# Kernel optimization log

Measured on AMD Instinct MI355X. Metric: run time of the kernel, lower is better.

## Reference

```python
import jax, jax.numpy as jnp
import numpy as np

# Config (matches init_kwargs)
V = 32000      # vocab_size
H = 1024       # hidden_size
NH = 16        # num_heads
NKV = 4        # num_kv_heads
L = 4          # num_layers
FF = 4096      # intermediate_size
MAXPOS = 2048
HD = H // NH   # head_dim = 64
KVD = H * NKV // NH  # kv projection dim = 256
EPS = 1e-5


def setup_inputs() -> dict:
    key = jax.random.key(0)
    ks = iter(jax.random.split(key, 64))
    B, T = 1, 2048
    std = 0.02

    def w(shape):
        return jax.random.normal(next(ks), shape, dtype=jnp.float32) * std

    inp = {
        "input_ids": jax.random.randint(next(ks), (B, T), 0, V),
        "attention_mask": jnp.zeros((B, T), dtype=jnp.float32),
        "tok_emb": w((V, H)),
        "pos_emb": w((MAXPOS, H)),
        # stacked per-layer params; Linear weights stored as [in, out]
        "qW": w((L, H, H)),   "qb": jnp.zeros((L, H)),
        "kW": w((L, H, KVD)), "kb": jnp.zeros((L, KVD)),
        "vW": w((L, H, KVD)), "vb": jnp.zeros((L, KVD)),
        "oW": w((L, H, H)),   "ob": jnp.zeros((L, H)),
        "m1W": w((L, H, FF)), "m1b": jnp.zeros((L, FF)),
        "m2W": w((L, FF, H)), "m2b": jnp.zeros((L, H)),
        "ln1g": jnp.ones((L, H)), "ln1b": jnp.zeros((L, H)),
        "ln2g": jnp.ones((L, H)), "ln2b": jnp.zeros((L, H)),
        "lnfg": jnp.ones((H,)),   "lnfb": jnp.zeros((H,)),
        "headW": w((H, V)),  # head: Linear(H, V, bias=False), stored [in,out]
    }
    return inp


def _layer_norm(x, g, b):
    m = jnp.mean(x, axis=-1, keepdims=True)
    v = jnp.mean(jnp.square(x - m), axis=-1, keepdims=True)
    return (x - m) * jax.lax.rsqrt(v + EPS) * g + b


def _gqa_attn(x, mask, qW, qb, kW, kb, vW, vb, oW, ob):
    B, T, _ = x.shape
    G = NH // NKV  # query groups per kv head
    q = (x @ qW + qb).reshape(B, T, NH, HD).transpose(0, 2, 1, 3)        # [B,NH,T,HD]
    q = q.reshape(B, NKV, G, T, HD)                                      # [B,NKV,G,T,HD]
    k = (x @ kW + kb).reshape(B, T, NKV, HD).transpose(0, 2, 1, 3)       # [B,NKV,T,HD]
    v = (x @ vW + vb).reshape(B, T, NKV, HD).transpose(0, 2, 1, 3)       # [B,NKV,T,HD]
    # naive full score tensor [B,NKV,G,T,T] (as in the original module)
    scores = jnp.einsum("bkgqd,bksd->bkgqs", q, k) / jnp.sqrt(jnp.float32(HD))
    scores = scores + mask[:, None, None, None, :]  # additive mask over keys
    attn = jax.nn.softmax(scores, axis=-1)
    out = jnp.einsum("bkgqs,bksd->bkgqd", attn, v)                       # [B,NKV,G,T,HD]
    out = out.reshape(B, NH, T, HD).transpose(0, 2, 1, 3).reshape(B, T, H)
    return out @ oW + ob


def reference(input_ids, attention_mask, tok_emb, pos_emb,
              qW, qb, kW, kb, vW, vb, oW, ob,
              m1W, m1b, m2W, m2b,
              ln1g, ln1b, ln2g, ln2b, lnfg, lnfb, headW):
    B, T = input_ids.shape
    x = tok_emb[input_ids] + pos_emb[jnp.arange(T)][None, :, :]  # [B,T,H]
    for i in range(L):
        h = _layer_norm(x, ln1g[i], ln1b[i])
        x = x + _gqa_attn(h, attention_mask, qW[i], qb[i], kW[i], kb[i],
                          vW[i], vb[i], oW[i], ob[i])
        h = _layer_norm(x, ln2g[i], ln2b[i])
        h = jax.nn.gelu(h @ m1W[i] + m1b[i], approximate=False) @ m2W[i] + m2b[i]
        x = x + h
    x = _layer_norm(x, lnfg, lnfb)
    logits = x @ headW  # [B,T,V]
    return logits
```

## Files before the change

### kernel.cpp

```cpp
#include <hip/hip_runtime.h>
#include <stdint.h>
#include <math.h>

typedef __attribute__((ext_vector_type(8))) short bf16x8;
typedef __attribute__((ext_vector_type(4))) short bf16x4;
typedef __attribute__((ext_vector_type(4))) float f32x4;

__device__ __forceinline__ short f2bf(float f) {
  unsigned u = __builtin_bit_cast(unsigned, f);
  unsigned r = u + 0x7fffu + ((u >> 16) & 1u);
  return (short)(r >> 16);
}

__device__ __forceinline__ f32x4 mfma16(bf16x8 a, bf16x8 b, f32x4 c) {
  return __builtin_amdgcn_mfma_f32_16x16x32_bf16(a, b, c, 0, 0, 0);
}

__device__ __forceinline__ void gload16(const void* g, void* l) {
  __builtin_amdgcn_global_load_lds((const __attribute__((address_space(1))) void*)g,
                                   (__attribute__((address_space(3))) void*)l, 16, 0, 0);
}

__device__ __forceinline__ int swz(int row, int col) {
  return row * 64 + (((col >> 3) ^ (row & 7)) << 3) + (col & 7);
}

__global__ __launch_bounds__(256) void embed_k(const int* __restrict__ ids,
                                               const float* __restrict__ tok,
                                               const float* __restrict__ pos,
                                               float* __restrict__ x) {
  int row = blockIdx.x, t = threadIdx.x;
  int id = ids[row];
  const float4 a = *reinterpret_cast<const float4*>(tok + (size_t)id * 1024 + t * 4);
  const float4 b = *reinterpret_cast<const float4*>(pos + (size_t)row * 1024 + t * 4);
  float4 o = make_float4(a.x + b.x, a.y + b.y, a.z + b.z, a.w + b.w);
  *reinterpret_cast<float4*>(x + (size_t)row * 1024 + t * 4) = o;
}

__global__ __launch_bounds__(256) void ln_k(const float* __restrict__ x,
                                            const float* __restrict__ gw,
                                            const float* __restrict__ bw,
                                            short* __restrict__ out) {
  int row = blockIdx.x, t = threadIdx.x;
  const float4 v = *reinterpret_cast<const float4*>(x + (size_t)row * 1024 + t * 4);
  float s = v.x + v.y + v.z + v.w;
  float q = v.x * v.x + v.y * v.y + v.z * v.z + v.w * v.w;
#pragma unroll
  for (int o = 32; o > 0; o >>= 1) { s += __shfl_xor(s, o); q += __shfl_xor(q, o); }
  __shared__ float sh[8];
  int w = t >> 6;
  if ((t & 63) == 0) { sh[w] = s; sh[4 + w] = q; }
  __syncthreads();
  float ts = sh[0] + sh[1] + sh[2] + sh[3];
  float tq = sh[4] + sh[5] + sh[6] + sh[7];
  float mean = ts * (1.f / 1024.f);
  float var  = tq * (1.f / 1024.f) - mean * mean;
  float rstd = rsqrtf(var + 1e-5f);
  const float4 gv = *reinterpret_cast<const float4*>(gw + t * 4);
  const float4 bv = *reinterpret_cast<const float4*>(bw + t * 4);
  bf16x4 ov = { f2bf((v.x - mean) * rstd * gv.x + bv.x),
                f2bf((v.y - mean) * rstd * gv.y + bv.y),
                f2bf((v.z - mean) * rstd * gv.z + bv.z),
                f2bf((v.w - mean) * rstd * gv.w + bv.w) };
  *reinterpret_cast<bf16x4*>(out + (size_t)row * 1024 + t * 4) = ov;
}

__global__ __launch_bounds__(256) void tcvt_k(const float* __restrict__ W,
                                              short* __restrict__ Wt,
                                              int N, size_t inStride, size_t outStride,
                                              int rowOff, int ldOut, float scale) {
  __shared__ float T[128][68];
  const float* Win = W + blockIdx.z * inStride;
  short* Wout = Wt + blockIdx.z * outStride;
  const int n0 = blockIdx.x * 64, k0 = blockIdx.y * 128;
  const int t = threadIdx.x;
  const int nc = (t & 15) * 4, kr = t >> 4;
#pragma unroll
  for (int p = 0; p < 8; ++p) {
    const float4 v = *reinterpret_cast<const float4*>(Win + (size_t)(k0 + kr + 16 * p) * N + n0 + nc);
    T[kr + 16 * p][nc + 0] = v.x;
    T[kr + 16 * p][nc + 1] = v.y;
    T[kr + 16 * p][nc + 2] = v.z;
    T[kr + 16 * p][nc + 3] = v.w;
  }
  __syncthreads();
  const int n = t >> 2, ks = (t & 3) * 32;
  short tmp[32];
#pragma unroll
  for (int i = 0; i < 32; ++i) tmp[i] = f2bf(T[ks + i][n] * scale);
  short* op = Wout + (size_t)(rowOff + n0 + n) * ldOut + k0 + ks;
#pragma unroll
  for (int c = 0; c < 4; ++c)
    *reinterpret_cast<bf16x8*>(op + c * 8) = *reinterpret_cast<bf16x8*>(tmp + c * 8);
}

__global__ __launch_bounds__(256) void bqkv_k(const float* __restrict__ qb,
                                              const float* __restrict__ kb,
                                              const float* __restrict__ vb,
                                              float* __restrict__ o) {
  int l = blockIdx.y;
  int c = blockIdx.x * 256 + threadIdx.x;
  float v;
  if (c < 1024) v = qb[l * 1024 + c] * 0.125f;
  else if (c < 1280) v = kb[l * 256 + c - 1024];
  else v = vb[l * 256 + c - 1280];
  o[l * 1536 + c] = v;
}

__global__ __launch_bounds__(256) void vtr_k(const short* __restrict__ v, int vld,
                                             short* __restrict__ vt) {
  __shared__ short T[64][80];
  const int kvh = blockIdx.y;
  const int s0 = blockIdx.x * 64;
  const int t = threadIdx.x;
  const int row = t >> 3, ch = t & 7;
#pragma unroll
  for (int p = 0; p < 2; ++p) {
    int s = row + 32 * p;
    bf16x8 vv = *reinterpret_cast<const bf16x8*>(v + (size_t)(s0 + s) * vld + kvh * 64 + ch * 8);
    *reinterpret_cast<bf16x8*>(&T[s][ch * 8]) = vv;
  }
  __syncthreads();
#pragma unroll
  for (int p = 0; p < 2; ++p) {
    int d = row + 32 * p;
    short tmp[8];
#pragma unroll
    for (int i = 0; i < 8; ++i) tmp[i] = T[ch * 8 + i][d];
    *reinterpret_cast<bf16x8*>(vt + (size_t)(kvh * 64 + d) * 2048 + s0 + ch * 8) =
        *reinterpret_cast<bf16x8*>(tmp);
  }
}

template <int EPI, int XSWZ, int TILE>
__global__ __launch_bounds__(256, 4)
void gemm_bt(const short* __restrict__ A, const short* __restrict__ Wt,
             const float* __restrict__ bias, const float* __restrict__ resid,
             void* __restrict__ out, int M, int N, int K, int nbOff,
             short* __restrict__ vt) {
  constexpr int BN   = (TILE == 0) ? 128 : 64;
  constexpr int WN   = (TILE == 0) ? 64 : 32;
  constexpr int NT   = (TILE == 0) ? 4 : 2;
  constexpr int BISS = (TILE == 0) ? 4 : 2;
  __shared__ short As[128 * 64];
  __shared__ short Bs[BN * 64];
  const int t = threadIdx.x;
  const int lane = t & 63, w = t >> 6;
  const int g = lane >> 4, r = lane & 15;
  const int wr = w >> 1, wc = w & 1;

  int bx = blockIdx.x, by = blockIdx.y;
  if (XSWZ == 1) {
    const int nbx = gridDim.x, nby = gridDim.y, nwg = nbx * nby;
    const int bid = by * nbx + bx;
    const int q = nwg >> 3, rr = nwg & 7;
    const int xcd = bid & 7, loc = bid >> 3;
    const int sw = (xcd < rr ? xcd * (q + 1) : rr * (q + 1) + (xcd - rr) * q) + loc;
    by = sw % nby; bx = sw / nby;
  }
  const int m0 = by * 128, n0 = (bx + nbOff) * BN;

  f32x4 acc[4][NT];
#pragma unroll
  for (int i = 0; i < 4; ++i)
#pragma unroll
    for (int j = 0; j < NT; ++j) { f32x4 z = {0.f, 0.f, 0.f, 0.f}; acc[i][j] = z; }

  const int srow = lane >> 3, sslot = lane & 7;

  for (int k0 = 0; k0 < K; k0 += 64) {
#pragma unroll
    for (int i = 0; i < 4; ++i) {
      const int rowA = w * 32 + i * 8 + srow;
      const int colA = (sslot ^ (srow & 7)) << 3;
      gload16(A + (size_t)(m0 + rowA) * K + k0 + colA, &As[(w * 32 + i * 8) * 64]);
    }
#pragma unroll
    for (int i = 0; i < BISS; ++i) {
      const int rowB = w * (8 * BISS) + i * 8 + srow;
      const int colB = (sslot ^ (srow & 7)) << 3;
      gload16(Wt + (size_t)(n0 + rowB) * K + k0 + colB, &Bs[(w * (8 * BISS) + i * 8) * 64]);
    }
    __syncthreads();
#pragma unroll
    for (int kk = 0; kk < 64; kk += 32) {
      bf16x8 af[4], bfg[NT];
#pragma unroll
      for (int mt = 0; mt < 4; ++mt)
        af[mt] = *reinterpret_cast<const bf16x8*>(&As[swz(wr * 64 + mt * 16 + r, kk + g * 8)]);
#pragma unroll
      for (int nt = 0; nt < NT; ++nt)
        bfg[nt] = *reinterpret_cast<const bf16x8*>(&Bs[swz(wc * WN + nt * 16 + r, kk + g * 8)]);
#pragma unroll
      for (int mt = 0; mt < 4; ++mt)
#pragma unroll
        for (int nt = 0; nt < NT; ++nt)
          acc[mt][nt] = mfma16(af[mt], bfg[nt], acc[mt][nt]);
    }
    __syncthreads();
  }
#pragma unroll
  for (int nt = 0; nt < NT; ++nt) {
    const int col = n0 + wc * WN + nt * 16 + r;
    const float bv = (EPI == 3) ? 0.f : bias[col];
#pragma unroll
    for (int mt = 0; mt < 4; ++mt) {
#pragma unroll
      for (int j = 0; j < 4; ++j) {
        const int row = m0 + wr * 64 + mt * 16 + 4 * g + j;
        const size_t oi = (size_t)row * N + col;
        float vv = acc[mt][nt][j] + bv;
        if (EPI == 0) {
          ((short*)out)[oi] = f2bf(vv);
        } else if (EPI == 1) {
          vv = 0.5f * vv * (1.f + erff(vv * 0.70710678118654752f));
          ((short*)out)[oi] = f2bf(vv);
        } else if (EPI == 2) {
          ((float*)out)[oi] = resid[oi] + vv;
        } else if (EPI == 3) {
          ((float*)out)[oi] = vv;
        } else {
          short bb = f2bf(vv);
          ((short*)out)[oi] = bb;
          if (col >= 1280) vt[(size_t)(col - 1280) * 2048 + row] = bb;
        }
      }
    }
  }
}

template <int EPI>
__global__ __launch_bounds__(256)
void gemm_k(const short* __restrict__ A, const float* __restrict__ W,
            const float* __restrict__ bias, const float* resid, void* out,
            int M, int N, int K, float scale) {
  __shared__ short As[128 * 64];
  __shared__ short Bs[128 * 64];
  const int t = threadIdx.x;
  const int lane = t & 63;
  const int g = lane >> 4, r = lane & 15;
  const int wid = t >> 6, wr = wid >> 1, wc = wid & 1;
  const int m0 = blockIdx.y * 128, n0 = blockIdx.x * 128;
  f32x4 acc[4][4];
#pragma unroll
  for (int i = 0; i < 4; ++i)
#pragma unroll
    for (int j = 0; j < 4; ++j) { f32x4 z = {0.f, 0.f, 0.f, 0.f}; acc[i][j] = z; }
  const int arow = t >> 3, ac = t & 7;
  const int bnn = t >> 1, bkh = t & 1;
  for (int k0 = 0; k0 < K; k0 += 64) {
#pragma unroll
    for (int p = 0; p < 4; ++p) {
      int row = arow + 32 * p;
      bf16x8 av = *reinterpret_cast<const bf16x8*>(A + (size_t)(m0 + row) * K + k0 + ac * 8);
      *reinterpret_cast<bf16x8*>(&As[swz(row, ac * 8)]) = av;
    }
#pragma unroll
    for (int p = 0; p < 8; ++p) {
      int kg = 4 * (bkh + 2 * p);
      const float* wp = W + (size_t)(k0 + kg) * N + n0 + bnn;
      bf16x4 wv = { f2bf(wp[0]), f2bf(wp[(size_t)N]), f2bf(wp[(size_t)2 * N]), f2bf(wp[(size_t)3 * N]) };
      *reinterpret_cast<bf16x4*>(&Bs[swz(bnn, kg)]) = wv;
    }
    __syncthreads();
#pragma unroll
    for (int kk = 0; kk < 64; kk += 32) {
      bf16x8 af[4], bfg[4];
#pragma unroll
      for (int mt = 0; mt < 4; ++mt)
        af[mt] = *reinterpret_cast<const bf16x8*>(&As[swz(wr * 64 + mt * 16 + r, kk + g * 8)]);
#pragma unroll
      for (int nt = 0; nt < 4; ++nt)
        bfg[nt] = *reinterpret_cast<const bf16x8*>(&Bs[swz(wc * 64 + nt * 16 + r, kk + g * 8)]);
#pragma unroll
      for (int mt = 0; mt < 4; ++mt)
#pragma unroll
        for (int nt = 0; nt < 4; ++nt)
          acc[mt][nt] = mfma16(af[mt], bfg[nt], acc[mt][nt]);
    }
    __syncthreads();
  }
#pragma unroll
  for (int nt = 0; nt < 4; ++nt) {
    const int col = n0 + wc * 64 + nt * 16 + r;
    const float bv = (EPI == 3) ? 0.f : bias[col];
#pragma unroll
    for (int mt = 0; mt < 4; ++mt) {
#pragma unroll
      for (int j = 0; j < 4; ++j) {
        const int row = m0 + wr * 64 + mt * 16 + 4 * g + j;
        const size_t oi = (size_t)row * N + col;
        float vv = acc[mt][nt][j] + bv;
        if (EPI == 0) {
          ((short*)out)[oi] = f2bf(vv * scale);
        } else if (EPI == 1) {
          vv = 0.5f * vv * (1.f + erff(vv * 0.70710678118654752f));
          ((short*)out)[oi] = f2bf(vv);
        } else if (EPI == 2) {
          ((float*)out)[oi] = resid[oi] + vv;
        } else {
          ((float*)out)[oi] = vv;
        }
      }
    }
  }
}

__global__ __launch_bounds__(256) void attn_k(const short* __restrict__ q, int qld,
                                              const short* __restrict__ k, int kld,
                                              const short* __restrict__ vt,
                                              const float* __restrict__ mask,
                                              short* __restrict__ o) {
  __shared__ short Ks[2][64 * 64];
  __shared__ short Vs[2][64 * 64];
  const int t = threadIdx.x, lane = t & 63, w = t >> 6;
  const int g = lane >> 4, r = lane & 15;
  const int h = blockIdx.y, qb = blockIdx.x, kvh = h >> 2;
  const int qrow = qb * 64 + w * 16 + r;

  const short* qp = q + (size_t)qrow * qld + h * 64;
  bf16x8 qf0 = *reinterpret_cast<const bf16x8*>(qp + g * 8);
  bf16x8 qf1 = *reinterpret_cast<const bf16x8*>(qp + 32 + g * 8);

  const short* kbase = k + kvh * 64;
  const short* vbase = vt + (size_t)kvh * 64 * 2048;

  f32x4 oacc[4];
#pragma unroll
  for (int i = 0; i < 4; ++i) { f32x4 z = {0.f, 0.f, 0.f, 0.f}; oacc[i] = z; }
  float m_run = -INFINITY, l_run = 0.f;

  const int srow = w * 8 + (lane >> 3), schunk = lane & 7;

#pragma unroll
  for (int p = 0; p < 2; ++p) {
    const int rr = srow + 32 * p;
    const int cc = (schunk ^ (rr & 7)) << 3;
    gload16(kbase + (size_t)rr * kld + cc, (char*)Ks + p * 4096 + w * 1024);
    gload16(vbase + (size_t)rr * 2048 + cc, (char*)Vs + p * 4096 + w * 1024);
  }
  asm volatile("s_waitcnt vmcnt(0)" ::: "memory");
  __syncthreads();

  for (int it = 0; it < 32; ++it) {
    const int cur = it & 1;
    if (it < 31) {
      const int s1 = (it + 1) * 64;
#pragma unroll
      for (int p = 0; p < 2; ++p) {
        const int rr = srow + 32 * p;
        const int cc = (schunk ^ (rr & 7)) << 3;
        gload16(kbase + (size_t)(s1 + rr) * kld + cc,
                (char*)Ks + (cur ^ 1) * 8192 + p * 4096 + w * 1024);
        gload16(vbase + (size_t)rr * 2048 + s1 + cc,
                (char*)Vs + (cur ^ 1) * 8192 + p * 4096 + w * 1024);
      }
    }
    const int s0 = it * 64;
    const short* Kc = Ks[cur];
    const short* Vc = Vs[cur];

    f32x4 sa[4];
#pragma unroll
    for (int st = 0; st < 4; ++st) {
      bf16x8 kf0 = *reinterpret_cast<const bf16x8*>(&Kc[swz(st * 16 + r, g * 8)]);
      bf16x8 kf1 = *reinterpret_cast<const bf16x8*>(&Kc[swz(st * 16 + r, 32 + g * 8)]);
      f32x4 z = {0.f, 0.f, 0.f, 0.f};
      z = mfma16(kf0, qf0, z);
      z = mfma16(kf1, qf1, z);
      sa[st] = z;
    }
    float sv[16];
    float pmax = -INFINITY;
#pragma unroll
    for (int st = 0; st < 4; ++st) {
      const float4 mv = *reinterpret_cast<const float4*>(mask + s0 + st * 16 + 4 * g);
#pragma unroll
      for (int j = 0; j < 4; ++j) {
        float xx = sa[st][j] + ((const float*)&mv)[j];
        sv[st * 4 + j] = xx;
        pmax = fmaxf(pmax, xx);
      }
    }
    pmax = fmaxf(pmax, __shfl_xor(pmax, 16));
    pmax = fmaxf(pmax, __shfl_xor(pmax, 32));
    float m_new = fmaxf(m_run, pmax);
    float corr = __expf(m_run - m_new);
    float psum = 0.f;
    short pb[16];
#pragma unroll
    for (int i = 0; i < 16; ++i) {
      float p = __expf(sv[i] - m_new);
      psum += p;
      pb[i] = f2bf(p);
    }
    psum += __shfl_xor(psum, 16);
    psum += __shfl_xor(psum, 32);
    l_run = l_run * corr + psum;
    m_run = m_new;
#pragma unroll
    for (int dt = 0; dt < 4; ++dt)
#pragma unroll
      for (int j = 0; j < 4; ++j) oacc[dt][j] *= corr;

#pragma unroll
    for (int hs = 0; hs < 2; ++hs) {
      bf16x8 pf = { pb[hs * 8 + 0], pb[hs * 8 + 1], pb[hs * 8 + 2], pb[hs * 8 + 3],
                    pb[hs * 8 + 4], pb[hs * 8 + 5], pb[hs * 8 + 6], pb[hs * 8 + 7] };
#pragma unroll
      for (int dt = 0; dt < 4; ++dt) {
        int d = dt * 16 + r;
        int c1 = 4 * g + 32 * hs;
        bf16x4 va  = *reinterpret_cast<const bf16x4*>(&Vc[swz(d, c1)]);
        bf16x4 vb2 = *reinterpret_cast<const bf16x4*>(&Vc[swz(d, c1 + 16)]);
        bf16x8 vf = { va[0], va[1], va[2], va[3], vb2[0], vb2[1], vb2[2], vb2[3] };
        oacc[dt] = mfma16(vf, pf, oacc[dt]);
      }
    }
    asm volatile("s_waitcnt vmcnt(0)" ::: "memory");
    __syncthreads();
  }
  float inv = 1.f / l_run;
#pragma unroll
  for (int dt = 0; dt < 4; ++dt) {
    bf16x4 ov = { f2bf(oacc[dt][0] * inv), f2bf(oacc[dt][1] * inv),
                  f2bf(oacc[dt][2] * inv), f2bf(oacc[dt][3] * inv) };
    *reinterpret_cast<bf16x4*>(o + (size_t)qrow * 1024 + h * 64 + dt * 16 + 4 * g) = ov;
  }
}

extern "C" void kernel_launch(void* const* d_in, const int* in_sizes, int n_in,
                              void* d_out, int out_size, void* d_ws, size_t ws_size,
                              hipStream_t stream) {
  const int*   ids   = (const int*)d_in[0];
  const float* mask  = (const float*)d_in[1];
  const float* tok   = (const float*)d_in[2];
  const float* pos   = (const float*)d_in[3];
  const float* qW    = (const float*)d_in[4];
  const float* qbias = (const float*)d_in[5];
  const float* kW    = (const float*)d_in[6];
  const float* kbias = (const float*)d_in[7];
  const float* vW    = (const float*)d_in[8];
  const float* vbias = (const float*)d_in[9];
  const float* oW    = (const float*)d_in[10];
  const float* obias = (const float*)d_in[11];
  const float* m1W   = (const float*)d_in[12];
  const float* m1b   = (const float*)d_in[13];
  const float* m2W   = (const float*)d_in[14];
  const float* m2b   = (const float*)d_in[15];
  const float* ln1g  = (const float*)d_in[16];
  const float* ln1b  = (const float*)d_in[17];
  const float* ln2g  = (const float*)d_in[18];
  const float* ln2b  = (const float*)d_in[19];
  const float* lnfg  = (const float*)d_in[20];
  const float* lnfb  = (const float*)d_in[21];
  const float* headW = (const float*)d_in[22];
  float* out = (float*)d_out;

  char* ws = (char*)d_ws;
  float* x   = (float*)ws;
  short* xb  = (short*)(ws + 8388608ull);

  const size_t OFF_QKV  = 12582912ull;
  const size_t OFF_AO   = 18874368ull;
  const size_t OFF_FF   = 23068672ull;
  const size_t OFF_BQ   = 39845888ull;
  const size_t OFF_WQKV = 39870464ull;
  const size_t OFF_WO   = 52453376ull;
  const size_t OFF_WM1  = 60841984ull;
  const size_t OFF_WM2  = 94396416ull;
  const size_t OFF_WH   = 127950848ull;
  const size_t NEED     = 193486848ull;

  if (ws_size >= NEED) {
    short* qkv  = (short*)(ws + OFF_QKV);
    short* ao   = (short*)(ws + OFF_AO);
    short* ff   = (short*)(ws + OFF_FF);
    short* vt   = ff;
    float* bqv  = (float*)(ws + OFF_BQ);
    short* Wqkv = (short*)(ws + OFF_WQKV);
    short* Wo   = (short*)(ws + OFF_WO);
    short* Wm1  = (short*)(ws + OFF_WM1);
    short* Wm2  = (short*)(ws + OFF_WM2);
    short* Wh   = (short*)(ws + OFF_WH);

    tcvt_k<<<dim3(16, 8, 4), 256, 0, stream>>>(qW, Wqkv, 1024, 1048576ull, 1572864ull, 0, 1024, 0.125f);
    tcvt_k<<<dim3(4, 8, 4),  256, 0, stream>>>(kW, Wqkv, 256,  262144ull,  1572864ull, 1024, 1024, 1.f);
    tcvt_k<<<dim3(4, 8, 4),  256, 0, stream>>>(vW, Wqkv, 256,  262144ull,  1572864ull, 1280, 1024, 1.f);
    tcvt_k<<<dim3(16, 8, 4), 256, 0, stream>>>(oW, Wo, 1024, 1048576ull, 1048576ull, 0, 1024, 1.f);
    tcvt_k<<<dim3(64, 8, 4), 256, 0, stream>>>(m1W, Wm1, 4096, 4194304ull, 4194304ull, 0, 1024, 1.f);
    tcvt_k<<<dim3(16, 32, 4), 256, 0, stream>>>(m2W, Wm2, 1024, 4194304ull, 4194304ull, 0, 4096, 1.f);
    tcvt_k<<<dim3(500, 8, 1), 256, 0, stream>>>(headW, Wh, 32000, 0ull, 0ull, 0, 1024, 1.f);
    bqkv_k<<<dim3(6, 4), 256, 0, stream>>>(qbias, kbias, vbias, bqv);

    embed_k<<<2048, 256, 0, stream>>>(ids, tok, pos, x);

    for (int l = 0; l < 4; ++l) {
      short* Wq_l  = Wqkv + (size_t)l * 1536 * 1024;
      short* Wo_l  = Wo   + (size_t)l * 1024 * 1024;
      short* Wm1_l = Wm1  + (size_t)l * 4096 * 1024;
      short* Wm2_l = Wm2  + (size_t)l * 1024 * 4096;

      ln_k<<<2048, 256, 0, stream>>>(x, ln1g + l * 1024, ln1b + l * 1024, xb);
      gemm_bt<4, 0, 1><<<dim3(24, 16), 256, 0, stream>>>(xb, Wq_l, bqv + l * 1536, nullptr,
                                                         qkv, 2048, 1536, 1024, 0, vt);
      attn_k<<<dim3(32, 16), 256, 0, stream>>>(qkv, 1536, qkv + 1024, 1536, vt, mask, ao);
      gemm_bt<2, 0, 1><<<dim3(16, 16), 256, 0, stream>>>(ao, Wo_l, obias + l * 1024, x,
                                                         x, 2048, 1024, 1024, 0, nullptr);
      ln_k<<<2048, 256, 0, stream>>>(x, ln2g + l * 1024, ln2b + l * 1024, xb);
      gemm_bt<1, 1, 0><<<dim3(32, 16), 256, 0, stream>>>(xb, Wm1_l, m1b + l * 4096, nullptr,
                                                         ff, 2048, 4096, 1024, 0, nullptr);
      gemm_bt<2, 1, 1><<<dim3(16, 16), 256, 0, stream>>>(ff, Wm2_l, m2b + l * 1024, x,
                                                         x, 2048, 1024, 4096, 0, nullptr);
    }
    ln_k<<<2048, 256, 0, stream>>>(x, lnfg, lnfb, xb);
    gemm_bt<3, 1, 0><<<dim3(250, 16), 256, 0, stream>>>(xb, Wh, nullptr, nullptr,
                                                        out, 2048, 32000, 1024, 0, nullptr);
  } else {
    short* qbf = (short*)(ws + (12u << 20));
    short* kbf = (short*)(ws + (16u << 20));
    short* vbf = (short*)(ws + (17u << 20));
    short* ao  = (short*)(ws + (18u << 20));
    short* ff  = (short*)(ws + (22u << 20));
    short* vtf = (short*)(ws + (38u << 20));

    embed_k<<<2048, 256, 0, stream>>>(ids, tok, pos, x);
    for (int l = 0; l < 4; ++l) {
      ln_k<<<2048, 256, 0, stream>>>(x, ln1g + l * 1024, ln1b + l * 1024, xb);
      gemm_k<0><<<dim3(8, 16), 256, 0, stream>>>(xb, qW + (size_t)l * 1024 * 1024,
          qbias + l * 1024, nullptr, qbf, 2048, 1024, 1024, 0.125f);
      gemm_k<0><<<dim3(2, 16), 256, 0, stream>>>(xb, kW + (size_t)l * 1024 * 256,
          kbias + l * 256, nullptr, kbf, 2048, 256, 1024, 1.f);
      gemm_k<0><<<dim3(2, 16), 256, 0, stream>>>(xb, vW + (size_t)l * 1024 * 256,
          vbias + l * 256, nullptr, vbf, 2048, 256, 1024, 1.f);
      vtr_k<<<dim3(32, 4), 256, 0, stream>>>(vbf, 256, vtf);
      attn_k<<<dim3(32, 16), 256, 0, stream>>>(qbf, 1024, kbf, 256, vtf, mask, ao);
      gemm_k<2><<<dim3(8, 16), 256, 0, stream>>>(ao, oW + (size_t)l * 1024 * 1024,
          obias + l * 1024, x, x, 2048, 1024, 1024, 1.f);
      ln_k<<<2048, 256, 0, stream>>>(x, ln2g + l * 1024, ln2b + l * 1024, xb);
      gemm_k<1><<<dim3(32, 16), 256, 0, stream>>>(xb, m1W + (size_t)l * 1024 * 4096,
          m1b + l * 4096, nullptr, ff, 2048, 4096, 1024, 1.f);
      gemm_k<2><<<dim3(8, 16), 256, 0, stream>>>(ff, m2W + (size_t)l * 4096 * 1024,
          m2b + l * 1024, x, x, 2048, 1024, 4096, 1.f);
    }
    ln_k<<<2048, 256, 0, stream>>>(x, lnfg, lnfb, xb);
    gemm_k<3><<<dim3(250, 16), 256, 0, stream>>>(xb, headW, nullptr, nullptr, out,
        2048, 32000, 1024, 1.f);
  }
}
```

Measured before the change: 1.191 ms.

## Use one wave per row in LN/embed, vectorize V-transpose stores, retile MLP1 and head GEMMs

LayerNorm and embedding now process four rows per block with one wavefront per row, which removes the shared-memory reduction and the block barrier. The QKV GEMM epilogue packs four bf16 values into one vector store for the transposed V buffer instead of doing scalar scattered stores. The MLP1 GEMM switches to a narrower-tile template with twice as many blocks, and the vocab head GEMM is split into two launches of half the grid using a column offset argument. The retiling trades per-block data reuse for more parallelism, and the split head adds one extra launch.

```diff
diff --git a/kernel.cpp b/kernel.cpp
--- a/kernel.cpp
+++ b/kernel.cpp
@@ -29,40 +29,49 @@
                                                const float* __restrict__ tok,
                                                const float* __restrict__ pos,
                                                float* __restrict__ x) {
-  int row = blockIdx.x, t = threadIdx.x;
-  int id = ids[row];
-  const float4 a = *reinterpret_cast<const float4*>(tok + (size_t)id * 1024 + t * 4);
-  const float4 b = *reinterpret_cast<const float4*>(pos + (size_t)row * 1024 + t * 4);
-  float4 o = make_float4(a.x + b.x, a.y + b.y, a.z + b.z, a.w + b.w);
-  *reinterpret_cast<float4*>(x + (size_t)row * 1024 + t * 4) = o;
+  const int t = threadIdx.x, w = t >> 6, lane = t & 63;
+  const int row = blockIdx.x * 4 + w;
+  const int id = ids[row];
+#pragma unroll
+  for (int i = 0; i < 4; ++i) {
+    const int c = (i * 64 + lane) * 4;
+    const float4 a = *reinterpret_cast<const float4*>(tok + (size_t)id * 1024 + c);
+    const float4 b = *reinterpret_cast<const float4*>(pos + (size_t)row * 1024 + c);
+    float4 o = make_float4(a.x + b.x, a.y + b.y, a.z + b.z, a.w + b.w);
+    *reinterpret_cast<float4*>(x + (size_t)row * 1024 + c) = o;
+  }
 }
 
 __global__ __launch_bounds__(256) void ln_k(const float* __restrict__ x,
                                             const float* __restrict__ gw,
                                             const float* __restrict__ bw,
                                             short* __restrict__ out) {
-  int row = blockIdx.x, t = threadIdx.x;
-  const float4 v = *reinterpret_cast<const float4*>(x + (size_t)row * 1024 + t * 4);
-  float s = v.x + v.y + v.z + v.w;
-  float q = v.x * v.x + v.y * v.y + v.z * v.z + v.w * v.w;
+  const int t = threadIdx.x, w = t >> 6, lane = t & 63;
+  const int row = blockIdx.x * 4 + w;
+  float4 v[4];
+  float s = 0.f, q = 0.f;
+#pragma unroll
+  for (int i = 0; i < 4; ++i) {
+    v[i] = *reinterpret_cast<const float4*>(x + (size_t)row * 1024 + (i * 64 + lane) * 4);
+    s += v[i].x + v[i].y + v[i].z + v[i].w;
+    q += v[i].x * v[i].x + v[i].y * v[i].y + v[i].z * v[i].z + v[i].w * v[i].w;
+  }
 #pragma unroll
   for (int o = 32; o > 0; o >>= 1) { s += __shfl_xor(s, o); q += __shfl_xor(q, o); }
-  __shared__ float sh[8];
-  int w = t >> 6;
-  if ((t & 63) == 0) { sh[w] = s; sh[4 + w] = q; }
-  __syncthreads();
-  float ts = sh[0] + sh[1] + sh[2] + sh[3];
-  float tq = sh[4] + sh[5] + sh[6] + sh[7];
-  float mean = ts * (1.f / 1024.f);
-  float var  = tq * (1.f / 1024.f) - mean * mean;
-  float rstd = rsqrtf(var + 1e-5f);
-  const float4 gv = *reinterpret_cast<const float4*>(gw + t * 4);
-  const float4 bv = *reinterpret_cast<const float4*>(bw + t * 4);
-  bf16x4 ov = { f2bf((v.x - mean) * rstd * gv.x + bv.x),
-                f2bf((v.y - mean) * rstd * gv.y + bv.y),
-                f2bf((v.z - mean) * rstd * gv.z + bv.z),
-                f2bf((v.w - mean) * rstd * gv.w + bv.w) };
-  *reinterpret_cast<bf16x4*>(out + (size_t)row * 1024 + t * 4) = ov;
+  const float mean = s * (1.f / 1024.f);
+  const float var  = q * (1.f / 1024.f) - mean * mean;
+  const float rstd = rsqrtf(var + 1e-5f);
+#pragma unroll
+  for (int i = 0; i < 4; ++i) {
+    const int c = (i * 64 + lane) * 4;
+    const float4 gv = *reinterpret_cast<const float4*>(gw + c);
+    const float4 bv = *reinterpret_cast<const float4*>(bw + c);
+    bf16x4 ov = { f2bf((v[i].x - mean) * rstd * gv.x + bv.x),
+                  f2bf((v[i].y - mean) * rstd * gv.y + bv.y),
+                  f2bf((v[i].z - mean) * rstd * gv.z + bv.z),
+                  f2bf((v[i].w - mean) * rstd * gv.w + bv.w) };
+    *reinterpret_cast<bf16x4*>(out + (size_t)row * 1024 + c) = ov;
+  }
 }
 
 __global__ __launch_bounds__(256) void tcvt_k(const float* __restrict__ W,
@@ -205,9 +214,11 @@
     const float bv = (EPI == 3) ? 0.f : bias[col];
 #pragma unroll
     for (int mt = 0; mt < 4; ++mt) {
+      const int rowb = m0 + wr * 64 + mt * 16 + 4 * g;
+      short vs[4];
 #pragma unroll
       for (int j = 0; j < 4; ++j) {
-        const int row = m0 + wr * 64 + mt * 16 + 4 * g + j;
+        const int row = rowb + j;
         const size_t oi = (size_t)row * N + col;
         float vv = acc[mt][nt][j] + bv;
         if (EPI == 0) {
@@ -222,8 +233,12 @@
         } else {
           short bb = f2bf(vv);
           ((short*)out)[oi] = bb;
-          if (col >= 1280) vt[(size_t)(col - 1280) * 2048 + row] = bb;
+          vs[j] = bb;
         }
+      }
+      if (EPI == 4 && col >= 1280) {
+        bf16x4 pk = { vs[0], vs[1], vs[2], vs[3] };
+        *reinterpret_cast<bf16x4*>(vt + (size_t)(col - 1280) * 2048 + rowb) = pk;
       }
     }
   }
@@ -493,7 +508,7 @@
     tcvt_k<<<dim3(500, 8, 1), 256, 0, stream>>>(headW, Wh, 32000, 0ull, 0ull, 0, 1024, 1.f);
     bqkv_k<<<dim3(6, 4), 256, 0, stream>>>(qbias, kbias, vbias, bqv);
 
-    embed_k<<<2048, 256, 0, stream>>>(ids, tok, pos, x);
+    embed_k<<<512, 256, 0, stream>>>(ids, tok, pos, x);
 
     for (int l = 0; l < 4; ++l) {
       short* Wq_l  = Wqkv + (size_t)l * 1536 * 1024;
@@ -501,21 +516,23 @@
       short* Wm1_l = Wm1  + (size_t)l * 4096 * 1024;
       short* Wm2_l = Wm2  + (size_t)l * 1024 * 4096;
 
-      ln_k<<<2048, 256, 0, stream>>>(x, ln1g + l * 1024, ln1b + l * 1024, xb);
+      ln_k<<<512, 256, 0, stream>>>(x, ln1g + l * 1024, ln1b + l * 1024, xb);
       gemm_bt<4, 0, 1><<<dim3(24, 16), 256, 0, stream>>>(xb, Wq_l, bqv + l * 1536, nullptr,
                                                          qkv, 2048, 1536, 1024, 0, vt);
       attn_k<<<dim3(32, 16), 256, 0, stream>>>(qkv, 1536, qkv + 1024, 1536, vt, mask, ao);
       gemm_bt<2, 0, 1><<<dim3(16, 16), 256, 0, stream>>>(ao, Wo_l, obias + l * 1024, x,
                                                          x, 2048, 1024, 1024, 0, nullptr);
-      ln_k<<<2048, 256, 0, stream>>>(x, ln2g + l * 1024, ln2b + l * 1024, xb);
-      gemm_bt<1, 1, 0><<<dim3(32, 16), 256, 0, stream>>>(xb, Wm1_l, m1b + l * 4096, nullptr,
+      ln_k<<<512, 256, 0, stream>>>(x, ln2g + l * 1024, ln2b + l * 1024, xb);
+      gemm_bt<1, 1, 1><<<dim3(64, 16), 256, 0, stream>>>(xb, Wm1_l, m1b + l * 4096, nullptr,
                                                          ff, 2048, 4096, 1024, 0, nullptr);
       gemm_bt<2, 1, 1><<<dim3(16, 16), 256, 0, stream>>>(ff, Wm2_l, m2b + l * 1024, x,
                                                          x, 2048, 1024, 4096, 0, nullptr);
     }
-    ln_k<<<2048, 256, 0, stream>>>(x, lnfg, lnfb, xb);
-    gemm_bt<3, 1, 0><<<dim3(250, 16), 256, 0, stream>>>(xb, Wh, nullptr, nullptr,
+    ln_k<<<512, 256, 0, stream>>>(x, lnfg, lnfb, xb);
+    gemm_bt<3, 1, 0><<<dim3(125, 16), 256, 0, stream>>>(xb, Wh, nullptr, nullptr,
                                                         out, 2048, 32000, 1024, 0, nullptr);
+    gemm_bt<3, 1, 0><<<dim3(125, 16), 256, 0, stream>>>(xb, Wh, nullptr, nullptr,
+                                                        out, 2048, 32000, 1024, 125, nullptr);
   } else {
     short* qbf = (short*)(ws + (12u << 20));
     short* kbf = (short*)(ws + (16u << 20));
@@ -524,9 +541,9 @@
     short* ff  = (short*)(ws + (22u << 20));
     short* vtf = (short*)(ws + (38u << 20));
 
-    embed_k<<<2048, 256, 0, stream>>>(ids, tok, pos, x);
+    embed_k<<<512, 256, 0, stream>>>(ids, tok, pos, x);
     for (int l = 0; l < 4; ++l) {
-      ln_k<<<2048, 256, 0, stream>>>(x, ln1g + l * 1024, ln1b + l * 1024, xb);
+      ln_k<<<512, 256, 0, stream>>>(x, ln1g + l * 1024, ln1b + l * 1024, xb);
       gemm_k<0><<<dim3(8, 16), 256, 0, stream>>>(xb, qW + (size_t)l * 1024 * 1024,
           qbias + l * 1024, nullptr, qbf, 2048, 1024, 1024, 0.125f);
       gemm_k<0><<<dim3(2, 16), 256, 0, stream>>>(xb, kW + (size_t)l * 1024 * 256,
@@ -537,13 +554,13 @@
       attn_k<<<dim3(32, 16), 256, 0, stream>>>(qbf, 1024, kbf, 256, vtf, mask, ao);
       gemm_k<2><<<dim3(8, 16), 256, 0, stream>>>(ao, oW + (size_t)l * 1024 * 1024,
           obias + l * 1024, x, x, 2048, 1024, 1024, 1.f);
-      ln_k<<<2048, 256, 0, stream>>>(x, ln2g + l * 1024, ln2b + l * 1024, xb);
+      ln_k<<<512, 256, 0, stream>>>(x, ln2g + l * 1024, ln2b + l * 1024, xb);
       gemm_k<1><<<dim3(32, 16), 256, 0, stream>>>(xb, m1W + (size_t)l * 1024 * 4096,
           m1b + l * 4096, nullptr, ff, 2048, 4096, 1024, 1.f);
       gemm_k<2><<<dim3(8, 16), 256, 0, stream>>>(ff, m2W + (size_t)l * 4096 * 1024,
           m2b + l * 1024, x, x, 2048, 1024, 4096, 1.f);
     }
-    ln_k<<<2048, 256, 0, stream>>>(x, lnfg, lnfb, xb);
+    ln_k<<<512, 256, 0, stream>>>(x, lnfg, lnfb, xb);
     gemm_k<3><<<dim3(250, 16), 256, 0, stream>>>(xb, headW, nullptr, nullptr, out,
         2048, 32000, 1024, 1.f);
   }
```

After: 1.176 ms. No clear change (-1.3%).
